# Kernel optimization log

Hardware: AMD Instinct MI355X
Metric: run time of the kernel (lower is better)

The kernel has to match this reference:

```python
import jax, jax.numpy as jnp
import numpy as np

HIDDEN = 1024
HEADS = 16
HEAD_DIM = HIDDEN // HEADS


def setup_inputs() -> dict:
    key = jax.random.key(0)
    ks = jax.random.split(key, 4)
    B, S, H = 2, 2048, HIDDEN
    scale = 1.0 / np.sqrt(H)
    return {
        "inputs": jax.random.normal(ks[0], (B, S, H), dtype=jnp.float32),
        "mask": jnp.ones((B, S), dtype=jnp.int32),
        "Wq": jax.random.normal(ks[1], (H, H), dtype=jnp.float32) * scale,
        "bq": jnp.zeros((H,), dtype=jnp.float32),
        "Wk": jax.random.normal(ks[2], (H, H), dtype=jnp.float32) * scale,
        "bk": jnp.zeros((H,), dtype=jnp.float32),
        "Wv": jax.random.normal(ks[3], (H, H), dtype=jnp.float32) * scale,
        "bv": jnp.zeros((H,), dtype=jnp.float32),
    }


def _split_heads(x, B, S):
    # [B,S,H] -> [B,heads,S,head_dim]
    return x.reshape(B, S, HEADS, HEAD_DIM).transpose(0, 2, 1, 3)


def reference(inputs, mask, Wq, bq, Wk, bk, Wv, bv):
    B, S, H = inputs.shape
    q = _split_heads(inputs @ Wq.T + bq, B, S)
    k = _split_heads(inputs @ Wk.T + bk, B, S)
    v = _split_heads(inputs @ Wv.T + bv, B, S)
    scores = jnp.einsum("bhqd,bhkd->bhqk", q, k) / jnp.sqrt(
        jnp.asarray(HEAD_DIM, dtype=inputs.dtype))
    # mask broadcast [B,1,1,S]; zeros -> -inf
    scores = jnp.where(mask[:, None, None, :] == 0, -jnp.inf, scores)
    attn = jax.nn.softmax(scores, axis=-1)
    context = jnp.einsum("bhqk,bhkd->bhqd", attn, v)
    return context.transpose(0, 2, 1, 3).reshape(B, S, H)
```

## Files before the change

### kernel.cpp

```cpp
#include <hip/hip_runtime.h>
#include <hip/hip_fp16.h>

constexpr int S_LEN  = 2048;
constexpr int HID    = 1024;
constexpr int HEADS  = 16;
constexpr int HDIM   = 64;
constexpr int BATCH  = 2;
constexpr int BH     = BATCH * HEADS;
constexpr int M_ROWS = BATCH * S_LEN;

typedef _Float16 half8  __attribute__((ext_vector_type(8)));
typedef _Float16 half4v __attribute__((ext_vector_type(4)));
typedef _Float16 half2v __attribute__((ext_vector_type(2)));
typedef float    f32x4  __attribute__((ext_vector_type(4)));
typedef float    f32x16 __attribute__((ext_vector_type(16)));
typedef unsigned uint4v __attribute__((ext_vector_type(4)));

constexpr float EXP2_OFF = -11.541560327111707f;
constexpr float Q_SCALE  = 0.18033688011112042f;

__global__ __launch_bounds__(256) void cvt_kernel(
    const float* __restrict__ X,  const float* __restrict__ Wq,
    const float* __restrict__ Wk, const float* __restrict__ Wv,
    const int* __restrict__ mask,
    _Float16* __restrict__ Xh,  _Float16* __restrict__ Wqh,
    _Float16* __restrict__ Wkh, _Float16* __restrict__ Wvh,
    float* __restrict__ maskF)
{
    const int blk = blockIdx.x;
    if (blk >= 3584) {
        const int loc = blk - 3584;
        const size_t e = ((size_t)loc * 256 + threadIdx.x) * 8;
        #pragma unroll
        for (int i = 0; i < 8; ++i)
            maskF[e + i] = mask[e + i] ? EXP2_OFF : -1.0e30f;
        return;
    }
    const float* src; _Float16* dst; int loc;
    if (blk < 2048)      { src = X;  dst = Xh;  loc = blk; }
    else if (blk < 2560) { src = Wq; dst = Wqh; loc = blk - 2048; }
    else if (blk < 3072) { src = Wk; dst = Wkh; loc = blk - 2560; }
    else                 { src = Wv; dst = Wvh; loc = blk - 3072; }
    const size_t e = ((size_t)loc * 256 + threadIdx.x) * 8;
    float4 a = *reinterpret_cast<const float4*>(&src[e]);
    float4 b = *reinterpret_cast<const float4*>(&src[e + 4]);
    half8 h = { (_Float16)a.x, (_Float16)a.y, (_Float16)a.z, (_Float16)a.w,
                (_Float16)b.x, (_Float16)b.y, (_Float16)b.z, (_Float16)b.w };
    *reinterpret_cast<half8*>(&dst[e]) = h;
}

__device__ __forceinline__ void async_cp16(_Float16* lds, const _Float16* g) {
    __builtin_amdgcn_global_load_lds(
        (const __attribute__((address_space(1))) void*)g,
        (__attribute__((address_space(3))) void*)lds, 16, 0, 0);
}
__device__ __forceinline__ void async_cp4(float* lds, const float* g) {
    __builtin_amdgcn_global_load_lds(
        (const __attribute__((address_space(1))) void*)g,
        (__attribute__((address_space(3))) void*)lds, 4, 0, 0);
}

__device__ __forceinline__ void permlane32_swap(unsigned &x, unsigned &y) {
    asm("v_permlane32_swap_b32 %0, %1" : "+v"(x), "+v"(y));
}

__global__ __launch_bounds__(256) void qkv_proj_kernel(
    const _Float16* __restrict__ Xh,
    const _Float16* __restrict__ Wqh, const _Float16* __restrict__ Wkh,
    const _Float16* __restrict__ Wvh,
    const float* __restrict__ bq, const float* __restrict__ bk,
    const float* __restrict__ bv,
    _Float16* __restrict__ Qo, _Float16* __restrict__ Ko,
    _Float16* __restrict__ Vt)
{
    const int mode = blockIdx.z;
    const _Float16* W    = (mode == 0) ? Wqh : (mode == 1) ? Wkh : Wvh;
    const float*    bias = (mode == 0) ? bq  : (mode == 1) ? bk  : bv;

    const int m0 = blockIdx.x * 128, n0 = blockIdx.y * 128;
    const int tid = threadIdx.x, wave = tid >> 6, lane = tid & 63;
    const int l31 = lane & 31, kg = lane >> 5;

    __shared__ _Float16 SMEM[24576];

    f32x16 acc[2][2];
    #pragma unroll
    for (int mt = 0; mt < 2; ++mt)
        #pragma unroll
        for (int nt = 0; nt < 2; ++nt)
            #pragma unroll
            for (int i = 0; i < 16; ++i) acc[mt][nt][i] = 0.f;

    const int wm = (wave & 1) * 64, wn = (wave >> 1) * 64;

    const int srow = tid >> 2, spos = tid & 3;
    auto stage = [&](int k0, int b) {
        _Float16* Asb = SMEM + b * 8192;
        _Float16* Bsb = Asb + 4096;
        #pragma unroll
        for (int j = 0; j < 2; ++j) {
            const int row = srow + j * 64;
            const int sch = spos ^ (row & 3);
            async_cp16(&Asb[j * 2048 + tid * 8],
                       &Xh[(size_t)(m0 + row) * HID + k0 + sch * 8]);
            async_cp16(&Bsb[j * 2048 + tid * 8],
                       &W [(size_t)(n0 + row) * HID + k0 + sch * 8]);
        }
    };

    constexpr int NIT = HID / 32;
    stage(0, 0);
    stage(32, 1);
    int buf = 0;

    for (int it = 0; it < NIT; ++it) {
        asm volatile("s_waitcnt vmcnt(4)" ::: "memory");
        __builtin_amdgcn_s_barrier();
        asm volatile("" ::: "memory");

        {
            int it2 = it + 2; if (it2 >= NIT) it2 -= NIT;
            int nb  = buf + 2; if (nb >= 3) nb -= 3;
            stage(it2 * 32, nb);
        }

        _Float16* Asb = SMEM + buf * 8192;
        _Float16* Bsb = Asb + 4096;

        #pragma unroll
        for (int c = 0; c < 2; ++c) {
            const int k8 = c * 2 + kg;
            half8 af[2], bf[2];
            #pragma unroll
            for (int mt = 0; mt < 2; ++mt) {
                const int row = wm + mt * 32 + l31;
                af[mt] = *reinterpret_cast<const half8*>(
                    &Asb[row * 32 + ((k8 ^ (row & 3)) * 8)]);
            }
            #pragma unroll
            for (int nt = 0; nt < 2; ++nt) {
                const int row = wn + nt * 32 + l31;
                bf[nt] = *reinterpret_cast<const half8*>(
                    &Bsb[row * 32 + ((k8 ^ (row & 3)) * 8)]);
            }
            __builtin_amdgcn_s_setprio(1);
            #pragma unroll
            for (int mt = 0; mt < 2; ++mt)
                #pragma unroll
                for (int nt = 0; nt < 2; ++nt)
                    acc[mt][nt] = __builtin_amdgcn_mfma_f32_32x32x16_f16(
                        af[mt], bf[nt], acc[mt][nt], 0, 0, 0);
            __builtin_amdgcn_s_setprio(0);
        }
        if (++buf == 3) buf = 0;
    }
    asm volatile("s_waitcnt vmcnt(0)" ::: "memory");
    __syncthreads();

    _Float16* T = SMEM + wave * 4608;

    const int nn  = n0 + wn;
    const int hh  = nn >> 6;
    const int mm  = m0 + wm;
    const int bb  = mm >> 11;
    const int bhv = bb * HEADS + hh;
    const int s0  = mm & 2047;
    const int rowg = lane >> 3, chunk = lane & 7;

    if (mode < 2) {
        _Float16* Out = (mode == 0) ? Qo : Ko;
        #pragma unroll
        for (int nt = 0; nt < 2; ++nt) {
            const int col = nt * 32 + l31;
            float bias_n = bias[nn + col];
            #pragma unroll
            for (int mt = 0; mt < 2; ++mt)
                #pragma unroll
                for (int r = 0; r < 16; ++r) {
                    const int row_l = (r & 3) + 8 * (r >> 2) + 4 * kg;
                    float v = acc[mt][nt][r] + bias_n;
                    if (mode == 0) v *= Q_SCALE;
                    T[(mt * 32 + row_l) * 72 + col] = (_Float16)v;
                }
        }
        asm volatile("s_waitcnt lgkmcnt(0)" ::: "memory");
        #pragma unroll
        for (int j = 0; j < 8; ++j) {
            const int sr = j * 8 + rowg;
            half8 v = *reinterpret_cast<const half8*>(&T[sr * 72 + chunk * 8]);
            *reinterpret_cast<half8*>(
                &Out[((size_t)bhv * S_LEN + s0 + sr) * HDIM + chunk * 8]) = v;
        }
    } else {
        #pragma unroll
        for (int nt = 0; nt < 2; ++nt) {
            const int col = nt * 32 + l31;
            const float bias_n = bias[nn + col];
            #pragma unroll
            for (int mt = 0; mt < 2; ++mt)
                #pragma unroll
                for (int rg = 0; rg < 4; ++rg) {
                    half4v t = { (_Float16)(acc[mt][nt][rg * 4 + 0] + bias_n),
                                 (_Float16)(acc[mt][nt][rg * 4 + 1] + bias_n),
                                 (_Float16)(acc[mt][nt][rg * 4 + 2] + bias_n),
                                 (_Float16)(acc[mt][nt][rg * 4 + 3] + bias_n) };
                    const int s_off = mt * 32 + 8 * rg + 4 * kg;
                    *reinterpret_cast<half4v*>(&T[col * 72 + s_off]) = t;
                }
        }
        asm volatile("s_waitcnt lgkmcnt(0)" ::: "memory");
        #pragma unroll
        for (int j = 0; j < 8; ++j) {
            const int dr = j * 8 + rowg;
            half8 v = *reinterpret_cast<const half8*>(&T[dr * 72 + chunk * 8]);
            *reinterpret_cast<half8*>(
                &Vt[((size_t)bhv * HDIM + dr) * S_LEN + s0 + chunk * 8]) = v;
        }
    }
}

__global__ __launch_bounds__(512, 4) void attn_kernel(
    const _Float16* __restrict__ Q, const _Float16* __restrict__ K,
    const _Float16* __restrict__ Vt, const float* __restrict__ maskF,
    float* __restrict__ Out)
{
    const int id   = blockIdx.x;
    const int xcd  = id & 7;
    const int bh   = xcd * 4 + ((id >> 3) & 3);
    const int qt   = id >> 5;
    const int b = bh >> 4, h = bh & 15;
    const int tid = threadIdx.x, wave = tid >> 6, lane = tid & 63;
    const int l31 = lane & 31, kg = lane >> 5;
    const int wq = wave & 3, wk = wave >> 2;

    __shared__ _Float16 SMEM[3 * 8192];
    __shared__ float    Ms[3][8][64];

    const _Float16* Qb = Q  + (size_t)bh * S_LEN * HDIM;
    const _Float16* Kb = K  + (size_t)bh * S_LEN * HDIM;
    const _Float16* Vb = Vt + (size_t)bh * HDIM * S_LEN;
    const float*    mb = maskF + b * S_LEN;

    const int qrow = qt * 128 + wq * 32 + l31;

    half8 qf[4];
    #pragma unroll
    for (int kc = 0; kc < 4; ++kc)
        qf[kc] = *reinterpret_cast<const half8*>(
            &Qb[(size_t)qrow * HDIM + kc * 16 + kg * 8]);
    asm volatile("s_waitcnt vmcnt(0)" ::: "memory");

    f32x16 acc[2];
    #pragma unroll
    for (int dt = 0; dt < 2; ++dt)
        #pragma unroll
        for (int i = 0; i < 16; ++i) acc[dt][i] = 0.f;
    float den = 0.f;

    const int srow = tid >> 3;
    const int slot = tid & 7;
    const int gs   = (srow + (srow >> 3)) & 7;
    auto stage = [&](int tile, int bufsel) {
        const int kb   = tile * 64;
        const int csrc = slot ^ gs;
        _Float16* Kd = SMEM + bufsel * 8192;
        async_cp16(&Kd[tid * 8], &Kb[(size_t)(kb + srow) * HDIM + csrc * 8]);
        async_cp16(&Kd[4096 + tid * 8],
                   &Vb[(size_t)srow * S_LEN + kb + csrc * 8]);
        async_cp4(&Ms[bufsel][wave][lane], &mb[kb + lane]);
    };

    constexpr int NT = S_LEN / 64;
    stage(0, 0);
    stage(1, 1);
    int buf = 0;
    const int gkey = (l31 + (l31 >> 3) + 4 * wk) & 7;
    const int gv0  = (l31 + (l31 >> 3)) & 7;
    const int gv1  = (gv0 + 4) & 7;

    for (int t = 0; t < NT; ++t) {
        asm volatile("s_waitcnt vmcnt(3)" ::: "memory");
        __builtin_amdgcn_s_barrier();
        asm volatile("" ::: "memory");

        {
            int nt2 = t + 2; if (nt2 >= NT) nt2 -= NT;
            int nb  = buf + 2; if (nb >= 3) nb -= 3;
            stage(nt2, nb);
        }

        const _Float16* Kl = SMEM + buf * 8192;
        const _Float16* Vl = Kl + 4096;
        const float*    Mw = Ms[buf][wave];

        float4 mm0 = *reinterpret_cast<const float4*>(&Mw[wk * 32 + 0 + kg * 4]);
        float4 mm1 = *reinterpret_cast<const float4*>(&Mw[wk * 32 + 8 + kg * 4]);
        float4 mm2 = *reinterpret_cast<const float4*>(&Mw[wk * 32 + 16 + kg * 4]);
        float4 mm3 = *reinterpret_cast<const float4*>(&Mw[wk * 32 + 24 + kg * 4]);
        f32x16 sc = { mm0.x, mm0.y, mm0.z, mm0.w,
                      mm1.x, mm1.y, mm1.z, mm1.w,
                      mm2.x, mm2.y, mm2.z, mm2.w,
                      mm3.x, mm3.y, mm3.z, mm3.w };

        const _Float16* Krow = &Kl[(wk * 32 + l31) * 64];
        half8 kf[4];
        #pragma unroll
        for (int kc = 0; kc < 4; ++kc)
            kf[kc] = *reinterpret_cast<const half8*>(
                &Krow[((kc * 2 + kg) ^ gkey) * 8]);
        __builtin_amdgcn_s_setprio(1);
        #pragma unroll
        for (int kc = 0; kc < 4; ++kc)
            sc = __builtin_amdgcn_mfma_f32_32x32x16_f16(kf[kc], qf[kc], sc, 0, 0, 0);
        __builtin_amdgcn_s_setprio(0);

        half8 vf[2][2];
        #pragma unroll
        for (int dt = 0; dt < 2; ++dt) {
            const _Float16* Vrow = &Vl[(dt * 32 + l31) * 64];
            const int gv = dt ? gv1 : gv0;
            #pragma unroll
            for (int hh = 0; hh < 2; ++hh)
                vf[dt][hh] = *reinterpret_cast<const half8*>(
                    &Vrow[((wk * 4 + hh * 2 + kg) ^ gv) * 8]);
        }

        float p[16];
        #pragma unroll
        for (int r = 0; r < 16; ++r)
            p[r] = __builtin_amdgcn_exp2f(sc[r]);
        den += (((p[0] + p[1]) + (p[2] + p[3])) +
                ((p[4] + p[5]) + (p[6] + p[7]))) +
               (((p[8] + p[9]) + (p[10] + p[11])) +
                ((p[12] + p[13]) + (p[14] + p[15])));

        #pragma unroll
        for (int hh = 0; hh < 2; ++hh) {
            unsigned a0 = __builtin_bit_cast(unsigned,
                __builtin_amdgcn_cvt_pkrtz(p[hh * 8 + 0], p[hh * 8 + 1]));
            unsigned a1 = __builtin_bit_cast(unsigned,
                __builtin_amdgcn_cvt_pkrtz(p[hh * 8 + 2], p[hh * 8 + 3]));
            unsigned b0 = __builtin_bit_cast(unsigned,
                __builtin_amdgcn_cvt_pkrtz(p[hh * 8 + 4], p[hh * 8 + 5]));
            unsigned b1 = __builtin_bit_cast(unsigned,
                __builtin_amdgcn_cvt_pkrtz(p[hh * 8 + 6], p[hh * 8 + 7]));
            permlane32_swap(a0, b0);
            permlane32_swap(a1, b1);
            uint4v pd = { a0, a1, b0, b1 };
            half8 pf = __builtin_bit_cast(half8, pd);
            __builtin_amdgcn_s_setprio(1);
            acc[0] = __builtin_amdgcn_mfma_f32_32x32x16_f16(
                vf[0][hh], pf, acc[0], 0, 0, 0);
            acc[1] = __builtin_amdgcn_mfma_f32_32x32x16_f16(
                vf[1][hh], pf, acc[1], 0, 0, 0);
            __builtin_amdgcn_s_setprio(0);
        }
        if (++buf == 3) buf = 0;
    }

    asm volatile("s_waitcnt vmcnt(0)" ::: "memory");
    __syncthreads();

    den += __shfl_xor(den, 32, 64);

    float* LF = reinterpret_cast<float*>(SMEM);
    float* DF = reinterpret_cast<float*>(Ms);
    if (wk == 1) {
        float* wbase = LF + (wq * 64 + lane) * 36;
        #pragma unroll
        for (int dt = 0; dt < 2; ++dt)
            #pragma unroll
            for (int g = 0; g < 4; ++g) {
                float4 o = { acc[dt][g * 4 + 0], acc[dt][g * 4 + 1],
                             acc[dt][g * 4 + 2], acc[dt][g * 4 + 3] };
                *reinterpret_cast<float4*>(&wbase[dt * 16 + g * 4]) = o;
            }
        if (kg == 0) DF[wq * 32 + l31] = den;
    }
    __syncthreads();
    if (wk == 0) {
        const float* rbase = LF + (wq * 64 + lane) * 36;
        const float inv = 1.0f / (den + DF[wq * 32 + l31]);
        float* orow = Out + ((size_t)(b * S_LEN + qrow)) * HID + h * HDIM;
        #pragma unroll
        for (int dt = 0; dt < 2; ++dt)
            #pragma unroll
            for (int g = 0; g < 4; ++g) {
                float4 pv = *reinterpret_cast<const float4*>(
                    &rbase[dt * 16 + g * 4]);
                float4 o = { (acc[dt][g * 4 + 0] + pv.x) * inv,
                             (acc[dt][g * 4 + 1] + pv.y) * inv,
                             (acc[dt][g * 4 + 2] + pv.z) * inv,
                             (acc[dt][g * 4 + 3] + pv.w) * inv };
                *reinterpret_cast<float4*>(&orow[dt * 32 + g * 8 + kg * 4]) = o;
            }
    }
}

extern "C" void kernel_launch(void* const* d_in, const int* in_sizes, int n_in,
                              void* d_out, int out_size, void* d_ws, size_t ws_size,
                              hipStream_t stream) {
    const float* X  = (const float*)d_in[0];
    const int*   mk = (const int*)  d_in[1];
    const float* Wq = (const float*)d_in[2];
    const float* bq = (const float*)d_in[3];
    const float* Wk = (const float*)d_in[4];
    const float* bk = (const float*)d_in[5];
    const float* Wv = (const float*)d_in[6];
    const float* bv = (const float*)d_in[7];
    float* out = (float*)d_out;

    _Float16* Xh  = (_Float16*)d_ws;
    _Float16* Wqh = Xh  + (size_t)M_ROWS * HID;
    _Float16* Wkh = Wqh + (size_t)HID * HID;
    _Float16* Wvh = Wkh + (size_t)HID * HID;
    _Float16* Q   = Wvh + (size_t)HID * HID;
    _Float16* K   = Q   + (size_t)BH * S_LEN * HDIM;
    _Float16* Vt  = K   + (size_t)BH * S_LEN * HDIM;
    float*    maskF = (float*)(Vt + (size_t)BH * S_LEN * HDIM);

    cvt_kernel<<<3586, 256, 0, stream>>>(X, Wq, Wk, Wv, mk, Xh, Wqh, Wkh, Wvh, maskF);

    dim3 gp(M_ROWS / 128, HID / 128, 3);
    qkv_proj_kernel<<<gp, 256, 0, stream>>>(Xh, Wqh, Wkh, Wvh, bq, bk, bv, Q, K, Vt);

    attn_kernel<<<512, 512, 0, stream>>>(Q, K, Vt, maskF, out);
}
```

Baseline: 171.3 us.

## Software-pipeline attention loop to overlap QK MFMA with previous tile's softmax-PV

Splits the per-tile attention body into a QK-score stage and a softmax/PV stage, then reorders the loop so the QK MFMAs and V fragment loads for tile t are issued before the exp2, pack and PV MFMAs for tile t-1. The aim is to hide MFMA latency and the transcendental/VALU work of the softmax behind independent matrix work. The cost is more live registers for the carried score accumulator and V fragments, which may reduce occupancy or cause spills. Buffer indexing now uses modulo arithmetic on t instead of a rotating counter.

```diff
diff --git a/kernel.cpp b/kernel.cpp
--- a/kernel.cpp
+++ b/kernel.cpp
@@ -271,36 +271,23 @@
     };
 
     constexpr int NT = S_LEN / 64;
-    stage(0, 0);
-    stage(1, 1);
-    int buf = 0;
     const int gkey = (l31 + (l31 >> 3) + 4 * wk) & 7;
     const int gv0  = (l31 + (l31 >> 3)) & 7;
     const int gv1  = (gv0 + 4) & 7;
 
-    for (int t = 0; t < NT; ++t) {
-        asm volatile("s_waitcnt vmcnt(3)" ::: "memory");
-        __builtin_amdgcn_s_barrier();
-        asm volatile("" ::: "memory");
-
-        {
-            int nt2 = t + 2; if (nt2 >= NT) nt2 -= NT;
-            int nb  = buf + 2; if (nb >= 3) nb -= 3;
-            stage(nt2, nb);
-        }
-
-        const _Float16* Kl = SMEM + buf * 8192;
+    auto qk_tile = [&](int bufsel, f32x16& scOut, half8 (&vfOut)[2][2]) {
+        const _Float16* Kl = SMEM + bufsel * 8192;
         const _Float16* Vl = Kl + 4096;
-        const float*    Mw = Ms[buf][wave];
+        const float*    Mw = Ms[bufsel][wave];
 
         float4 mm0 = *reinterpret_cast<const float4*>(&Mw[wk * 32 + 0 + kg * 4]);
         float4 mm1 = *reinterpret_cast<const float4*>(&Mw[wk * 32 + 8 + kg * 4]);
         float4 mm2 = *reinterpret_cast<const float4*>(&Mw[wk * 32 + 16 + kg * 4]);
         float4 mm3 = *reinterpret_cast<const float4*>(&Mw[wk * 32 + 24 + kg * 4]);
-        f32x16 sc = { mm0.x, mm0.y, mm0.z, mm0.w,
-                      mm1.x, mm1.y, mm1.z, mm1.w,
-                      mm2.x, mm2.y, mm2.z, mm2.w,
-                      mm3.x, mm3.y, mm3.z, mm3.w };
+        scOut = (f32x16){ mm0.x, mm0.y, mm0.z, mm0.w,
+                          mm1.x, mm1.y, mm1.z, mm1.w,
+                          mm2.x, mm2.y, mm2.z, mm2.w,
+                          mm3.x, mm3.y, mm3.z, mm3.w };
 
         const _Float16* Krow = &Kl[(wk * 32 + l31) * 64];
         half8 kf[4];
@@ -311,24 +298,26 @@
         __builtin_amdgcn_s_setprio(1);
         #pragma unroll
         for (int kc = 0; kc < 4; ++kc)
-            sc = __builtin_amdgcn_mfma_f32_32x32x16_f16(kf[kc], qf[kc], sc, 0, 0, 0);
+            scOut = __builtin_amdgcn_mfma_f32_32x32x16_f16(
+                kf[kc], qf[kc], scOut, 0, 0, 0);
         __builtin_amdgcn_s_setprio(0);
 
-        half8 vf[2][2];
         #pragma unroll
         for (int dt = 0; dt < 2; ++dt) {
             const _Float16* Vrow = &Vl[(dt * 32 + l31) * 64];
             const int gv = dt ? gv1 : gv0;
             #pragma unroll
             for (int hh = 0; hh < 2; ++hh)
-                vf[dt][hh] = *reinterpret_cast<const half8*>(
+                vfOut[dt][hh] = *reinterpret_cast<const half8*>(
                     &Vrow[((wk * 4 + hh * 2 + kg) ^ gv) * 8]);
         }
-
+    };
+
+    auto finish_tile = [&](const f32x16& scP, const half8 (&vfP)[2][2]) {
         float p[16];
         #pragma unroll
         for (int r = 0; r < 16; ++r)
-            p[r] = __builtin_amdgcn_exp2f(sc[r]);
+            p[r] = __builtin_amdgcn_exp2f(scP[r]);
         den += (((p[0] + p[1]) + (p[2] + p[3])) +
                 ((p[4] + p[5]) + (p[6] + p[7]))) +
                (((p[8] + p[9]) + (p[10] + p[11])) +
@@ -350,13 +339,48 @@
             half8 pf = __builtin_bit_cast(half8, pd);
             __builtin_amdgcn_s_setprio(1);
             acc[0] = __builtin_amdgcn_mfma_f32_32x32x16_f16(
-                vf[0][hh], pf, acc[0], 0, 0, 0);
+                vfP[0][hh], pf, acc[0], 0, 0, 0);
             acc[1] = __builtin_amdgcn_mfma_f32_32x32x16_f16(
-                vf[1][hh], pf, acc[1], 0, 0, 0);
+                vfP[1][hh], pf, acc[1], 0, 0, 0);
             __builtin_amdgcn_s_setprio(0);
         }
-        if (++buf == 3) buf = 0;
-    }
+    };
+
+    stage(0, 0);
+    stage(1, 1);
+
+    f32x16 scP;
+    half8  vfP[2][2];
+    asm volatile("s_waitcnt vmcnt(3)" ::: "memory");
+    __builtin_amdgcn_s_barrier();
+    asm volatile("" ::: "memory");
+    stage(2, 2);
+    qk_tile(0, scP, vfP);
+
+    for (int t = 1; t < NT; ++t) {
+        asm volatile("s_waitcnt vmcnt(3)" ::: "memory");
+        __builtin_amdgcn_s_barrier();
+        asm volatile("" ::: "memory");
+
+        {
+            int nt2 = t + 2; if (nt2 >= NT) nt2 -= NT;
+            int nb  = t + 2; nb -= (nb / 3) * 3;
+            stage(nt2, nb);
+        }
+
+        f32x16 scC;
+        half8  vfC[2][2];
+        qk_tile(t - (t / 3) * 3, scC, vfC);
+        finish_tile(scP, vfP);
+
+        scP = scC;
+        #pragma unroll
+        for (int dt = 0; dt < 2; ++dt)
+            #pragma unroll
+            for (int hh = 0; hh < 2; ++hh)
+                vfP[dt][hh] = vfC[dt][hh];
+    }
+    finish_tile(scP, vfP);
 
     asm volatile("s_waitcnt vmcnt(0)" ::: "memory");
     __syncthreads();
```

After: 242.8 us. +41.7%, slower.
